# Kernel optimization log

Measured on AMD Instinct MI355X. Metric: run time of the kernel, lower is better.

## Reference

```python
import jax, jax.numpy as jnp
import numpy as np

B, N, E, H, NDIM, WS = 1, 4096, 512, 8, 16, 128


def setup_inputs() -> dict:
    key = jax.random.key(0)
    ks = jax.random.split(key, 8)
    x = jax.random.normal(ks[0], (B, N, E), jnp.float32)
    W_qkv = jax.random.normal(ks[1], (E, 3 * E), jnp.float32) * (E ** -0.5)
    b_qkv = jnp.zeros((3 * E,), jnp.float32)
    W_out = jax.random.normal(ks[2], (E, E), jnp.float32) * (E ** -0.5)
    b_out = jnp.zeros((E,), jnp.float32)
    omega = jax.random.normal(ks[3], (E,), jnp.float32)
    p_coeff = 0.1 * jax.random.normal(ks[4], (E, NDIM), jnp.float32)
    # keep |q|<1 so the 4096-step EMA recurrence is stable (original randn init diverges)
    q_coeff = jax.random.uniform(ks[5], (E, NDIM), jnp.float32, minval=-0.95, maxval=0.95)
    gamma = 0.1 * jax.random.normal(ks[6], (E, NDIM), jnp.float32)
    adaptive_weights = jnp.ones((2,), jnp.float32)
    return dict(x=x, W_qkv=W_qkv, b_qkv=b_qkv, W_out=W_out, b_out=b_out,
                omega=omega, p_coeff=p_coeff, q_coeff=q_coeff, gamma=gamma,
                adaptive_weights=adaptive_weights)


def reference(x, W_qkv, b_qkv, W_out, b_out, omega, p_coeff, q_coeff, gamma, adaptive_weights):
    b, n, e = x.shape
    dk = e // H
    # qkv projection
    qkv = x @ W_qkv + b_qkv                                # (b, n, 3e)
    q, k, v = jnp.split(qkv, 3, axis=-1)
    to_heads = lambda t: t.reshape(b, n, H, dk).transpose(0, 2, 1, 3)  # (b, h, n, dk)
    q, k, v = to_heads(q), to_heads(k), to_heads(v)
    # full QK^T (as in source) then block-local causal multiplicative mask
    dots = jnp.einsum('bhid,bhjd->bhij', q, k) * (dk ** -0.5)
    idx = jnp.arange(n)
    blk, pos = idx // WS, idx % WS
    mask = (blk[:, None] == blk[None, :]) & (pos[None, :] <= pos[:, None])
    dots = dots * mask.astype(dots.dtype)                  # scores * tril within each window block, 0 elsewhere
    attn = jax.nn.softmax(dots, axis=-1)                   # dropout is identity in eval
    out_attn = jnp.einsum('bhij,bhjd->bhid', attn, v)
    out_attn = out_attn.transpose(0, 2, 1, 3).reshape(b, n, e) @ W_out + b_out
    # CEMA: per-channel linear recurrence h_t = p*x_t + q*h_{t-1}; y_t = sum_d gamma*h_t
    # (source uses complex64 hidden but p,q,gamma,x are real -> imag part stays 0; .real == real math)
    ndim = p_coeff.shape[1]
    def step(h, xt):                                       # h: (b, e, ndim), xt: (b, e)
        h = p_coeff[None] * xt[:, :, None] + q_coeff[None] * h
        return h, jnp.sum(gamma[None] * h, axis=-1)        # (b, e)
    h0 = jnp.zeros((b, e, ndim), x.dtype)
    _, ys = jax.lax.scan(step, h0, jnp.swapaxes(x, 0, 1))  # ys: (n, b, e)
    x_cema = jnp.swapaxes(ys, 0, 1)
    w = jax.nn.softmax(adaptive_weights)
    return w[0] * out_attn + w[1] * x_cema
```

## Files before the change

kernel.cpp:

```cpp
#include <hip/hip_runtime.h>
#include <hip/hip_bf16.h>


typedef __bf16 bf16x8 __attribute__((ext_vector_type(8)));
typedef float  f32x4  __attribute__((ext_vector_type(4)));

#define N_TOK   4096
#define EDIM    512
#define DKH     64
#define WSZ     128
#define QKV_LD  1536
#define CCH     128
#define CLEN    32

__device__ __forceinline__ void glds16(const void* gsrc, void* ldst) {
  __builtin_amdgcn_global_load_lds(
      (const __attribute__((address_space(1))) void*)gsrc,
      (__attribute__((address_space(3))) void*)ldst,
      16, 0, 0);
}

template <int MODE, int BM, int BN, int WM, int WN>
__device__ __forceinline__ void gemm_body(const __bf16* __restrict__ A,
                                          const __bf16* __restrict__ Bt,
                                          const float* __restrict__ bias,
                                          __bf16* __restrict__ Cb,
                                          float* __restrict__ Cf,
                                          int K, int ldc,
                                          const float* __restrict__ cema,
                                          const float* __restrict__ aw,
                                          int bx, int by, int t) {
  __shared__ __bf16 As[BM * 32];
  __shared__ __bf16 Bs[BN * 32];
  const int lane = t & 63, wid = t >> 6;
  const int quad = lane >> 4, c16 = lane & 15;
  const int wm = (wid % (BM / WM)) * WM, wn = (wid / (BM / WM)) * WN;
  const int m0 = bx * BM, n0 = by * BN;

  f32x4 acc[WM / 16][WN / 16] = {};

  const int ar = t >> 2, ac = (t & 3) * 8;
  const __bf16* gA = A + (size_t)(m0 + ar) * K + ac;
  const __bf16* gB = Bt + (size_t)(n0 + ar) * K + ac;

  for (int k0 = 0; k0 < K; k0 += 32) {
#pragma unroll
    for (int i = 0; i < BM / 64; i++)
      glds16(gA + (size_t)i * 64 * K + k0, As + i * 2048 + t * 8);
#pragma unroll
    for (int i = 0; i < BN / 64; i++)
      glds16(gB + (size_t)i * 64 * K + k0, Bs + i * 2048 + t * 8);
    __syncthreads();
    bf16x8 af[WM / 16], bf[WN / 16];
#pragma unroll
    for (int i = 0; i < WM / 16; i++)
      af[i] = *(const bf16x8*)&As[(wm + i * 16 + c16) * 32 + quad * 8];
#pragma unroll
    for (int i = 0; i < WN / 16; i++)
      bf[i] = *(const bf16x8*)&Bs[(wn + i * 16 + c16) * 32 + quad * 8];
#pragma unroll
    for (int mi = 0; mi < WM / 16; mi++)
#pragma unroll
      for (int ni = 0; ni < WN / 16; ni++)
        acc[mi][ni] = __builtin_amdgcn_mfma_f32_16x16x32_bf16(af[mi], bf[ni], acc[mi][ni], 0, 0, 0);
    __syncthreads();
  }

  float w0 = 1.f, w1 = 0.f;
  if (MODE == 1) {
    float a0 = aw[0], a1 = aw[1];
    float mx = fmaxf(a0, a1);
    float e0 = __expf(a0 - mx), e1 = __expf(a1 - mx);
    w0 = e0 / (e0 + e1);
    w1 = 1.f - w0;
  }
#pragma unroll
  for (int mi = 0; mi < WM / 16; mi++) {
#pragma unroll
    for (int ni = 0; ni < WN / 16; ni++) {
      const int col = n0 + wn + ni * 16 + c16;
      const float bv = bias[col];
#pragma unroll
      for (int r = 0; r < 4; r++) {
        const int row = m0 + wm + mi * 16 + quad * 4 + r;
        float v = acc[mi][ni][r] + bv;
        if (MODE == 1) {
          v = w0 * v + w1 * cema[(size_t)row * EDIM + col];
          Cf[(size_t)row * ldc + col] = v;
        } else {
          Cb[(size_t)row * ldc + col] = (__bf16)v;
        }
      }
    }
  }
}

__global__ __launch_bounds__(256) void fused_prep_cemaA(const float* __restrict__ Wq,
                                                        __bf16* __restrict__ WtQ,
                                                        const float* __restrict__ Wo,
                                                        __bf16* __restrict__ WtO,
                                                        const float* __restrict__ x,
                                                        const float* __restrict__ pc,
                                                        const float* __restrict__ qc,
                                                        float* __restrict__ h_end,
                                                        __bf16* __restrict__ x_bf,
                                                        float* __restrict__ xpart) {
  const int b = blockIdx.x, t = threadIdx.x;
  if (b < 256) {
    __shared__ float tile[64][65];
    int bx = b & 31;
    const int by = b >> 5;
    const float* in;
    __bf16* out;
    int C;
    if (bx < 24) { in = Wq; out = WtQ; C = 1536; }
    else         { bx -= 24; in = Wo; out = WtO; C = 512; }
    const int R = 512;
#pragma unroll
    for (int i = 0; i < 16; i++) {
      int idx = t + i * 256;
      int r = idx >> 6, c = idx & 63;
      tile[r][c] = in[(size_t)(by * 64 + r) * C + bx * 64 + c];
    }
    __syncthreads();
#pragma unroll
    for (int i = 0; i < 16; i++) {
      int idx = t + i * 256;
      int r = idx >> 6, c = idx & 63;
      out[(size_t)(bx * 64 + r) * R + by * 64 + c] = (__bf16)tile[c][r];
    }
  } else {
    const int bb = b - 256;
    const int c = bb >> 1;
    const int e = ((bb & 1) << 8) + t;
    float p[16], q[16], h[16];
#pragma unroll
    for (int d4 = 0; d4 < 4; d4++) {
      const float4 pv = ((const float4*)(pc + e * 16))[d4];
      const float4 qv = ((const float4*)(qc + e * 16))[d4];
      p[d4 * 4 + 0] = pv.x; p[d4 * 4 + 1] = pv.y; p[d4 * 4 + 2] = pv.z; p[d4 * 4 + 3] = pv.w;
      q[d4 * 4 + 0] = qv.x; q[d4 * 4 + 1] = qv.y; q[d4 * 4 + 2] = qv.z; q[d4 * 4 + 3] = qv.w;
    }
#pragma unroll
    for (int d = 0; d < 16; d++) h[d] = 0.f;
    const float* xp = x + (size_t)c * CLEN * EDIM + e;
    __bf16* xb = x_bf + (size_t)c * CLEN * EDIM + e;
    float sx = 0.f;
#pragma unroll 4
    for (int tt = 0; tt < CLEN; tt++) {
      const float xv = xp[(size_t)tt * EDIM];
      xb[(size_t)tt * EDIM] = (__bf16)xv;
      sx += xv;
#pragma unroll
      for (int d = 0; d < 16; d++) h[d] = fmaf(p[d], xv, q[d] * h[d]);
    }
    xpart[(size_t)c * 512 + e] = sx;
    float* o = h_end + (size_t)c * 8192 + e * 16;
#pragma unroll
    for (int d = 0; d < 16; d++) o[d] = h[d];
  }
}

__global__ __launch_bounds__(256) void fused_qkv_scan_vtot(const __bf16* __restrict__ x_bf,
                                                           const __bf16* __restrict__ WtQ,
                                                           const float* __restrict__ b_qkv,
                                                           __bf16* __restrict__ qkv,
                                                           const float* __restrict__ qc,
                                                           const float* __restrict__ h_end,
                                                           float* __restrict__ hin,
                                                           float* __restrict__ T,
                                                           const float* __restrict__ xpart,
                                                           float* __restrict__ vtot) {
  const int b = blockIdx.x, t = threadIdx.x;
  if (b < 384) {
    gemm_body<0, 128, 128, 64, 64>(x_bf, WtQ, b_qkv, qkv, nullptr,
                                   EDIM, QKV_LD, nullptr, nullptr,
                                   b & 31, b >> 5, t);
  } else if (b < 640) {
    const int idx = (b - 384) * 256 + t;
    const int g = idx >> 13;
    const int i = idx & 8191;
    const float q = qc[i];
    float Q = q * q; Q = Q * Q; Q = Q * Q; Q = Q * Q; Q = Q * Q;
    float L = 0.f;
    const int c0 = g * 16;
#pragma unroll 4
    for (int j = 0; j < 16; j++) {
      hin[(size_t)(c0 + j) * 8192 + i] = L;
      L = h_end[(size_t)(c0 + j) * 8192 + i] + Q * L;
    }
    T[(size_t)g * 8192 + i] = L;
  } else {
    __shared__ float xs[512];
    float s0 = 0.f, s1 = 0.f;
    for (int c = 0; c < CCH; c++) {
      s0 += xpart[(size_t)c * 512 + t];
      s1 += xpart[(size_t)c * 512 + 256 + t];
    }
    xs[t] = s0; xs[256 + t] = s1;
    __syncthreads();
    const int wid = t >> 6, lane = t & 63;
#pragma unroll
    for (int u = 0; u < 8; u++) {
      const int c = (b - 640) * 32 + wid * 8 + u;
      const bf16x8 wv = *(const bf16x8*)(WtQ + (size_t)(1024 + c) * 512 + lane * 8);
      float s = 0.f;
#pragma unroll
      for (int z = 0; z < 8; z++) s = fmaf((float)wv[z], xs[lane * 8 + z], s);
#pragma unroll
      for (int m = 1; m < 64; m <<= 1) s += __shfl_xor(s, m);
      if (lane == 0) vtot[c] = s + (float)N_TOK * b_qkv[1024 + c];
    }
  }
}

__global__ __launch_bounds__(256) void fused_attn_cemaC(const __bf16* __restrict__ qkv,
                                                        const float* __restrict__ vtot,
                                                        __bf16* __restrict__ out_attn,
                                                        const float* __restrict__ x,
                                                        const float* __restrict__ pc,
                                                        const float* __restrict__ qc,
                                                        const float* __restrict__ gma,
                                                        const float* __restrict__ hin,
                                                        const float* __restrict__ T,
                                                        float* __restrict__ y) {
  const int b = blockIdx.x, t = threadIdx.x;
  if (b < 256) {
    __shared__ float4 smem4[3104];
    __bf16* Qs = (__bf16*)smem4;
    __bf16* Ks = (__bf16*)smem4 + 8192;
    __bf16* Ws = (__bf16*)smem4;
    __bf16* Vt = (__bf16*)smem4 + 16384;
    float* rowsum = (float*)((__bf16*)smem4 + 24576);

    const int lane = t & 63, wid = t >> 6;
    const int quad = lane >> 4, c16 = lane & 15;
    const int h = b & 7, w = b >> 3;
    const size_t base = (size_t)w * WSZ * QKV_LD + h * DKH;

    const int sr = t >> 3, sc = (t & 7) * 8;
#pragma unroll
    for (int i = 0; i < 4; i++) {
      glds16(qkv + base + (size_t)(i * 32 + sr) * QKV_LD + sc,        Qs + i * 2048 + t * 8);
      glds16(qkv + base + EDIM + (size_t)(i * 32 + sr) * QKV_LD + sc, Ks + i * 2048 + t * 8);
    }
    __syncthreads();

    const int wm = (wid & 1) * 64, wn = (wid >> 1) * 64;
    f32x4 accs[4][4] = {};
#pragma unroll
    for (int k0 = 0; k0 < DKH; k0 += 32) {
      bf16x8 af[4], bf[4];
#pragma unroll
      for (int i = 0; i < 4; i++) {
        af[i] = *(const bf16x8*)&Qs[(wm + i * 16 + c16) * DKH + k0 + quad * 8];
        bf[i] = *(const bf16x8*)&Ks[(wn + i * 16 + c16) * DKH + k0 + quad * 8];
      }
#pragma unroll
      for (int mi = 0; mi < 4; mi++)
#pragma unroll
        for (int ni = 0; ni < 4; ni++)
          accs[mi][ni] = __builtin_amdgcn_mfma_f32_16x16x32_bf16(af[mi], bf[ni], accs[mi][ni], 0, 0, 0);
    }
    __syncthreads();

    if (t < 128) rowsum[t] = 0.f;
    __syncthreads();

#pragma unroll
    for (int mi = 0; mi < 4; mi++) {
      float rs[4] = {0.f, 0.f, 0.f, 0.f};
#pragma unroll
      for (int ni = 0; ni < 4; ni++) {
        const int j = wn + ni * 16 + c16;
#pragma unroll
        for (int r = 0; r < 4; r++) {
          const int i = wm + mi * 16 + quad * 4 + r;
          const float s = accs[mi][ni][r] * 0.125f;
          const float wv = (j <= i) ? (__expf(s) - 1.f) : 0.f;
          Ws[i * 128 + j] = (__bf16)wv;
          rs[r] += wv;
        }
      }
#pragma unroll
      for (int m = 1; m < 16; m <<= 1)
#pragma unroll
        for (int r = 0; r < 4; r++) rs[r] += __shfl_xor(rs[r], m);
      if (c16 == 0) {
#pragma unroll
        for (int r = 0; r < 4; r++)
          atomicAdd(&rowsum[wm + mi * 16 + quad * 4 + r], rs[r]);
      }
    }

    {
      const int j = t & 127;
      const int dh = (t >> 7) * 32;
      const __bf16* vp = qkv + base + 2 * EDIM + (size_t)j * QKV_LD + dh;
#pragma unroll
      for (int u = 0; u < 4; u++) {
        bf16x8 vv = *(const bf16x8*)(vp + u * 8);
#pragma unroll
        for (int x2 = 0; x2 < 8; x2++) Vt[(dh + u * 8 + x2) * 128 + j] = vv[x2];
      }
    }
    __syncthreads();

    f32x4 acco[2][4] = {};
#pragma unroll
    for (int j0 = 0; j0 < 128; j0 += 32) {
      bf16x8 af2[2], bf2[4];
#pragma unroll
      for (int mi = 0; mi < 2; mi++)
        af2[mi] = *(const bf16x8*)&Ws[(wid * 32 + mi * 16 + c16) * 128 + j0 + quad * 8];
#pragma unroll
      for (int ni = 0; ni < 4; ni++)
        bf2[ni] = *(const bf16x8*)&Vt[(ni * 16 + c16) * 128 + j0 + quad * 8];
#pragma unroll
      for (int mi = 0; mi < 2; mi++)
#pragma unroll
        for (int ni = 0; ni < 4; ni++)
          acco[mi][ni] = __builtin_amdgcn_mfma_f32_16x16x32_bf16(af2[mi], bf2[ni], acco[mi][ni], 0, 0, 0);
    }

#pragma unroll
    for (int mi = 0; mi < 2; mi++) {
#pragma unroll
      for (int ni = 0; ni < 4; ni++) {
        const int d = ni * 16 + c16;
        const float vt = vtot[h * DKH + d];
#pragma unroll
        for (int r = 0; r < 4; r++) {
          const int i = wid * 32 + mi * 16 + quad * 4 + r;
          const float denom = rowsum[i] + (float)N_TOK;
          const float val = (acco[mi][ni][r] + vt) / denom;
          out_attn[(size_t)(w * WSZ + i) * EDIM + h * DKH + d] = (__bf16)val;
        }
      }
    }
  } else {
    const int bb = b - 256;
    const int c = bb >> 1;
    const int e = ((bb & 1) << 8) + t;
    const int g = c >> 4, j = c & 15;
    float p[16], q[16], gm[16], h[16], Sv[16], Q32[16], Q512[16];
#pragma unroll
    for (int d4 = 0; d4 < 4; d4++) {
      const float4 pv = ((const float4*)(pc + e * 16))[d4];
      const float4 qv = ((const float4*)(qc + e * 16))[d4];
      const float4 gv = ((const float4*)(gma + e * 16))[d4];
      p[d4 * 4 + 0] = pv.x; p[d4 * 4 + 1] = pv.y; p[d4 * 4 + 2] = pv.z; p[d4 * 4 + 3] = pv.w;
      q[d4 * 4 + 0] = qv.x; q[d4 * 4 + 1] = qv.y; q[d4 * 4 + 2] = qv.z; q[d4 * 4 + 3] = qv.w;
      gm[d4 * 4 + 0] = gv.x; gm[d4 * 4 + 1] = gv.y; gm[d4 * 4 + 2] = gv.z; gm[d4 * 4 + 3] = gv.w;
    }
#pragma unroll
    for (int d = 0; d < 16; d++) {
      float Q = q[d] * q[d]; Q = Q * Q; Q = Q * Q; Q = Q * Q; Q = Q * Q;
      Q32[d] = Q;
      float Q5 = Q * Q; Q5 = Q5 * Q5; Q5 = Q5 * Q5; Q5 = Q5 * Q5;
      Q512[d] = Q5;
      Sv[d] = 0.f;
    }
    for (int gg = 0; gg < g; gg++) {
      const float* Tp = T + (size_t)gg * 8192 + e * 16;
#pragma unroll
      for (int d = 0; d < 16; d++) Sv[d] = Tp[d] + Q512[d] * Sv[d];
    }
    const float* hi = hin + (size_t)c * 8192 + e * 16;
#pragma unroll
    for (int d = 0; d < 16; d++) {
      float Qj = 1.f;
      for (int jj = 0; jj < j; jj++) Qj *= Q32[d];
      h[d] = hi[d] + Qj * Sv[d];
    }
    const float* xp = x + (size_t)c * CLEN * EDIM + e;
    float* yp = y + (size_t)c * CLEN * EDIM + e;
#pragma unroll 4
    for (int tt = 0; tt < CLEN; tt++) {
      const float xv = xp[(size_t)tt * EDIM];
      float acc = 0.f;
#pragma unroll
      for (int d = 0; d < 16; d++) {
        h[d] = fmaf(p[d], xv, q[d] * h[d]);
        acc = fmaf(gm[d], h[d], acc);
      }
      yp[(size_t)tt * EDIM] = acc;
    }
  }
}

__global__ __launch_bounds__(256) void gemm_out_kernel(const __bf16* __restrict__ A,
                                                       const __bf16* __restrict__ Bt,
                                                       const float* __restrict__ bias,
                                                       float* __restrict__ Cf,
                                                       const float* __restrict__ cema,
                                                       const float* __restrict__ aw) {
  gemm_body<1, 64, 64, 32, 32>(A, Bt, bias, nullptr, Cf, EDIM, EDIM, cema, aw,
                               blockIdx.x, blockIdx.y, threadIdx.x);
}

extern "C" void kernel_launch(void* const* d_in, const int* in_sizes, int n_in,
                              void* d_out, int out_size, void* d_ws, size_t ws_size,
                              hipStream_t stream) {
  const float* x       = (const float*)d_in[0];
  const float* W_qkv   = (const float*)d_in[1];
  const float* b_qkv   = (const float*)d_in[2];
  const float* W_out   = (const float*)d_in[3];
  const float* b_out   = (const float*)d_in[4];
  const float* p_coeff = (const float*)d_in[6];
  const float* q_coeff = (const float*)d_in[7];
  const float* gamma   = (const float*)d_in[8];
  const float* aw      = (const float*)d_in[9];

  char* ws = (char*)d_ws;
  __bf16* qkv      = (__bf16*)(ws);
  __bf16* WtQ      = (__bf16*)(ws + 12582912);
  __bf16* WtO      = (__bf16*)(ws + 14155776);
  __bf16* out_attn = (__bf16*)(ws + 14680064);
  float*  vtot     = (float*) (ws + 18874368);
  float*  h_end    = (float*) (ws + 18876416);
  float*  hin      = (float*) (ws + 23070720);
  float*  y        = (float*) (ws + 27265024);
  __bf16* x_bf     = (__bf16*)(ws + 35653632);
  float*  Tg       = (float*) (ws + 39849984);
  float*  xpart    = (float*) (ws + 40112128);

  fused_prep_cemaA<<<512, 256, 0, stream>>>(W_qkv, WtQ, W_out, WtO,
                                            x, p_coeff, q_coeff, h_end, x_bf, xpart);

  fused_qkv_scan_vtot<<<656, 256, 0, stream>>>(x_bf, WtQ, b_qkv, qkv,
                                               q_coeff, h_end, hin, Tg, xpart, vtot);

  fused_attn_cemaC<<<512, 256, 0, stream>>>(qkv, vtot, out_attn,
                                            x, p_coeff, q_coeff, gamma, hin, Tg, y);

  gemm_out_kernel<<<dim3(64, 8), 256, 0, stream>>>(out_attn, WtO, b_out,
                                                   (float*)d_out, y, aw);
}
```

Baseline: 125.9 us.

## Fuse QKV projection into windowed attention and fold vtot term into output GEMM

The QKV GEMM now runs inside the per-window, per-head attention block. Each 512-thread workgroup computes its Q/K/V tile straight into LDS and then does QK^T, the exp-1 weighting and PV, so the 12MB qkv buffer is never written to or read back from global memory. The constant softmax term (sum of V over all tokens) is moved out of attention: the CEMA kernel computes vtot·W_out per head, and the output GEMM adds it scaled by a per-row reciprocal denominator. The CEMA inter-chunk scan becomes a flat 128-step sequential pass, replacing the two-level T/Q512 prefix, and the GEMMs gain double-buffered LDS loads. The cost is a fused kernel with only 256 heavy blocks, each using large LDS, plus a longer serial scan path.

```diff
diff --git a/kernel.cpp b/kernel.cpp
--- a/kernel.cpp
+++ b/kernel.cpp
@@ -9,7 +9,6 @@
 #define EDIM    512
 #define DKH     64
 #define WSZ     128
-#define QKV_LD  1536
 #define CCH     128
 #define CLEN    32
 
@@ -18,81 +17,6 @@
       (const __attribute__((address_space(1))) void*)gsrc,
       (__attribute__((address_space(3))) void*)ldst,
       16, 0, 0);
-}
-
-template <int MODE, int BM, int BN, int WM, int WN>
-__device__ __forceinline__ void gemm_body(const __bf16* __restrict__ A,
-                                          const __bf16* __restrict__ Bt,
-                                          const float* __restrict__ bias,
-                                          __bf16* __restrict__ Cb,
-                                          float* __restrict__ Cf,
-                                          int K, int ldc,
-                                          const float* __restrict__ cema,
-                                          const float* __restrict__ aw,
-                                          int bx, int by, int t) {
-  __shared__ __bf16 As[BM * 32];
-  __shared__ __bf16 Bs[BN * 32];
-  const int lane = t & 63, wid = t >> 6;
-  const int quad = lane >> 4, c16 = lane & 15;
-  const int wm = (wid % (BM / WM)) * WM, wn = (wid / (BM / WM)) * WN;
-  const int m0 = bx * BM, n0 = by * BN;
-
-  f32x4 acc[WM / 16][WN / 16] = {};
-
-  const int ar = t >> 2, ac = (t & 3) * 8;
-  const __bf16* gA = A + (size_t)(m0 + ar) * K + ac;
-  const __bf16* gB = Bt + (size_t)(n0 + ar) * K + ac;
-
-  for (int k0 = 0; k0 < K; k0 += 32) {
-#pragma unroll
-    for (int i = 0; i < BM / 64; i++)
-      glds16(gA + (size_t)i * 64 * K + k0, As + i * 2048 + t * 8);
-#pragma unroll
-    for (int i = 0; i < BN / 64; i++)
-      glds16(gB + (size_t)i * 64 * K + k0, Bs + i * 2048 + t * 8);
-    __syncthreads();
-    bf16x8 af[WM / 16], bf[WN / 16];
-#pragma unroll
-    for (int i = 0; i < WM / 16; i++)
-      af[i] = *(const bf16x8*)&As[(wm + i * 16 + c16) * 32 + quad * 8];
-#pragma unroll
-    for (int i = 0; i < WN / 16; i++)
-      bf[i] = *(const bf16x8*)&Bs[(wn + i * 16 + c16) * 32 + quad * 8];
-#pragma unroll
-    for (int mi = 0; mi < WM / 16; mi++)
-#pragma unroll
-      for (int ni = 0; ni < WN / 16; ni++)
-        acc[mi][ni] = __builtin_amdgcn_mfma_f32_16x16x32_bf16(af[mi], bf[ni], acc[mi][ni], 0, 0, 0);
-    __syncthreads();
-  }
-
-  float w0 = 1.f, w1 = 0.f;
-  if (MODE == 1) {
-    float a0 = aw[0], a1 = aw[1];
-    float mx = fmaxf(a0, a1);
-    float e0 = __expf(a0 - mx), e1 = __expf(a1 - mx);
-    w0 = e0 / (e0 + e1);
-    w1 = 1.f - w0;
-  }
-#pragma unroll
-  for (int mi = 0; mi < WM / 16; mi++) {
-#pragma unroll
-    for (int ni = 0; ni < WN / 16; ni++) {
-      const int col = n0 + wn + ni * 16 + c16;
-      const float bv = bias[col];
-#pragma unroll
-      for (int r = 0; r < 4; r++) {
-        const int row = m0 + wm + mi * 16 + quad * 4 + r;
-        float v = acc[mi][ni][r] + bv;
-        if (MODE == 1) {
-          v = w0 * v + w1 * cema[(size_t)row * EDIM + col];
-          Cf[(size_t)row * ldc + col] = v;
-        } else {
-          Cb[(size_t)row * ldc + col] = (__bf16)v;
-        }
-      }
-    }
-  }
 }
 
 __global__ __launch_bounds__(256) void fused_prep_cemaA(const float* __restrict__ Wq,
@@ -161,189 +85,205 @@
   }
 }
 
-__global__ __launch_bounds__(256) void fused_qkv_scan_vtot(const __bf16* __restrict__ x_bf,
-                                                           const __bf16* __restrict__ WtQ,
-                                                           const float* __restrict__ b_qkv,
-                                                           __bf16* __restrict__ qkv,
-                                                           const float* __restrict__ qc,
-                                                           const float* __restrict__ h_end,
-                                                           float* __restrict__ hin,
-                                                           float* __restrict__ T,
-                                                           const float* __restrict__ xpart,
-                                                           float* __restrict__ vtot) {
-  const int b = blockIdx.x, t = threadIdx.x;
-  if (b < 384) {
-    gemm_body<0, 128, 128, 64, 64>(x_bf, WtQ, b_qkv, qkv, nullptr,
-                                   EDIM, QKV_LD, nullptr, nullptr,
-                                   b & 31, b >> 5, t);
-  } else if (b < 640) {
-    const int idx = (b - 384) * 256 + t;
-    const int g = idx >> 13;
-    const int i = idx & 8191;
+__global__ __launch_bounds__(512) void fused_qkv_attn_scanB(const __bf16* __restrict__ x_bf,
+                                                            const __bf16* __restrict__ WtQ,
+                                                            const float* __restrict__ b_qkv,
+                                                            const float* __restrict__ qc,
+                                                            const float* __restrict__ h_end,
+                                                            float* __restrict__ hin,
+                                                            __bf16* __restrict__ out_attn,
+                                                            float* __restrict__ rd) {
+  const int B = blockIdx.x, t = threadIdx.x;
+  __shared__ f32x4 smemv[3680];
+  if (B >= 256) {
+    const int i = (B - 256) * 512 + t;
     const float q = qc[i];
     float Q = q * q; Q = Q * Q; Q = Q * Q; Q = Q * Q; Q = Q * Q;
     float L = 0.f;
-    const int c0 = g * 16;
 #pragma unroll 4
-    for (int j = 0; j < 16; j++) {
-      hin[(size_t)(c0 + j) * 8192 + i] = L;
-      L = h_end[(size_t)(c0 + j) * 8192 + i] + Q * L;
-    }
-    T[(size_t)g * 8192 + i] = L;
-  } else {
-    __shared__ float xs[512];
-    float s0 = 0.f, s1 = 0.f;
-    for (int c = 0; c < CCH; c++) {
-      s0 += xpart[(size_t)c * 512 + t];
-      s1 += xpart[(size_t)c * 512 + 256 + t];
-    }
-    xs[t] = s0; xs[256 + t] = s1;
+    for (int c = 0; c < 128; c++) {
+      hin[(size_t)c * 8192 + i] = L;
+      L = h_end[(size_t)c * 8192 + i] + Q * L;
+    }
+    return;
+  }
+  char* sb = (char*)smemv;
+  const int lane = t & 63, wid = t >> 6;
+  const int quad = lane >> 4, c16 = lane & 15;
+  const int xcd = B & 7, h = (B >> 3) & 7, wg = B >> 6;
+  const int w = wg * 8 + xcd;
+
+  __bf16* AsP[2] = {(__bf16*)sb, (__bf16*)(sb + 20480)};
+  __bf16* BsP[2] = {(__bf16*)(sb + 8192), (__bf16*)(sb + 28672)};
+
+  const int wm = (wid & 3) * 32, wc = (wid >> 2) * 96;
+  f32x4 acc[2][6] = {};
+  const int ar = t >> 2, ac8 = (t & 3) * 8;
+  const __bf16* gA = x_bf + (size_t)(w * 128 + ar) * 512 + ac8;
+  const int grB0 = (ar < 64) ? (h * 64 + ar) : (512 + h * 64 + (ar - 64));
+  const __bf16* gB0 = WtQ + (size_t)grB0 * 512 + ac8;
+  const __bf16* gB1 = WtQ + (size_t)(1024 + h * 64 + ar) * 512 + ac8;
+
+  glds16(gA, AsP[0] + t * 8);
+  glds16(gB0, BsP[0] + t * 8);
+  if (wid < 4) glds16(gB1, BsP[0] + 4096 + t * 8);
+  __syncthreads();
+
+  int cur = 0;
+  for (int k0 = 0; k0 < 512; k0 += 32) {
+    if (k0 + 32 < 512) {
+      glds16(gA + k0 + 32, AsP[cur ^ 1] + t * 8);
+      glds16(gB0 + k0 + 32, BsP[cur ^ 1] + t * 8);
+      if (wid < 4) glds16(gB1 + k0 + 32, BsP[cur ^ 1] + 4096 + t * 8);
+    }
+    bf16x8 af[2], bfr[6];
+#pragma unroll
+    for (int i = 0; i < 2; i++)
+      af[i] = *(const bf16x8*)&AsP[cur][(wm + i * 16 + c16) * 32 + quad * 8];
+#pragma unroll
+    for (int j = 0; j < 6; j++)
+      bfr[j] = *(const bf16x8*)&BsP[cur][(wc + j * 16 + c16) * 32 + quad * 8];
+#pragma unroll
+    for (int mi = 0; mi < 2; mi++)
+#pragma unroll
+      for (int ni = 0; ni < 6; ni++)
+        acc[mi][ni] = __builtin_amdgcn_mfma_f32_16x16x32_bf16(af[mi], bfr[ni], acc[mi][ni], 0, 0, 0);
     __syncthreads();
-    const int wid = t >> 6, lane = t & 63;
-#pragma unroll
-    for (int u = 0; u < 8; u++) {
-      const int c = (b - 640) * 32 + wid * 8 + u;
-      const bf16x8 wv = *(const bf16x8*)(WtQ + (size_t)(1024 + c) * 512 + lane * 8);
-      float s = 0.f;
-#pragma unroll
-      for (int z = 0; z < 8; z++) s = fmaf((float)wv[z], xs[lane * 8 + z], s);
-#pragma unroll
-      for (int m = 1; m < 64; m <<= 1) s += __shfl_xor(s, m);
-      if (lane == 0) vtot[c] = s + (float)N_TOK * b_qkv[1024 + c];
-    }
-  }
-}
-
-__global__ __launch_bounds__(256) void fused_attn_cemaC(const __bf16* __restrict__ qkv,
-                                                        const float* __restrict__ vtot,
-                                                        __bf16* __restrict__ out_attn,
-                                                        const float* __restrict__ x,
-                                                        const float* __restrict__ pc,
-                                                        const float* __restrict__ qc,
-                                                        const float* __restrict__ gma,
-                                                        const float* __restrict__ hin,
-                                                        const float* __restrict__ T,
-                                                        float* __restrict__ y) {
+    cur ^= 1;
+  }
+
+  __bf16* Qs = (__bf16*)sb;
+  __bf16* Ks = (__bf16*)(sb + 18432);
+  __bf16* Vt = (__bf16*)(sb + 40960);
+  __bf16* Ws = (__bf16*)sb;
+  float* rowsum = (float*)(sb + 58368);
+
+#pragma unroll
+  for (int ni = 0; ni < 6; ni++) {
+    const int cc = wc + ni * 16 + c16;
+    const int g = cc >> 6;
+    const int d = cc & 63;
+    const float bv = b_qkv[g * 512 + h * 64 + d];
+#pragma unroll
+    for (int mi = 0; mi < 2; mi++)
+#pragma unroll
+      for (int r = 0; r < 4; r++) {
+        const int row = wm + mi * 16 + quad * 4 + r;
+        const float v = acc[mi][ni][r] + bv;
+        if (g == 0)      Qs[row * 72 + d] = (__bf16)v;
+        else if (g == 1) Ks[row * 72 + d] = (__bf16)v;
+        else             Vt[d * 136 + row] = (__bf16)v;
+      }
+  }
+  __syncthreads();
+
+  const int swm = (wid & 1) * 64, swn = (wid >> 1) * 32;
+  f32x4 accs[4][2] = {};
+#pragma unroll
+  for (int k0 = 0; k0 < DKH; k0 += 32) {
+    bf16x8 af2[4], bf2[2];
+#pragma unroll
+    for (int i = 0; i < 4; i++)
+      af2[i] = *(const bf16x8*)&Qs[(swm + i * 16 + c16) * 72 + k0 + quad * 8];
+#pragma unroll
+    for (int j = 0; j < 2; j++)
+      bf2[j] = *(const bf16x8*)&Ks[(swn + j * 16 + c16) * 72 + k0 + quad * 8];
+#pragma unroll
+    for (int mi = 0; mi < 4; mi++)
+#pragma unroll
+      for (int ni = 0; ni < 2; ni++)
+        accs[mi][ni] = __builtin_amdgcn_mfma_f32_16x16x32_bf16(af2[mi], bf2[ni], accs[mi][ni], 0, 0, 0);
+  }
+  __syncthreads();
+  if (t < 128) rowsum[t] = 0.f;
+  __syncthreads();
+
+#pragma unroll
+  for (int mi = 0; mi < 4; mi++) {
+    float rs[4] = {0.f, 0.f, 0.f, 0.f};
+#pragma unroll
+    for (int ni = 0; ni < 2; ni++) {
+      const int j = swn + ni * 16 + c16;
+#pragma unroll
+      for (int r = 0; r < 4; r++) {
+        const int i = swm + mi * 16 + quad * 4 + r;
+        const float s = accs[mi][ni][r] * 0.125f;
+        const float wv = (j <= i) ? (__expf(s) - 1.f) : 0.f;
+        Ws[i * 136 + j] = (__bf16)wv;
+        rs[r] += wv;
+      }
+    }
+#pragma unroll
+    for (int m = 1; m < 16; m <<= 1)
+#pragma unroll
+      for (int r = 0; r < 4; r++) rs[r] += __shfl_xor(rs[r], m);
+    if (c16 == 0) {
+#pragma unroll
+      for (int r = 0; r < 4; r++)
+        atomicAdd(&rowsum[swm + mi * 16 + quad * 4 + r], rs[r]);
+    }
+  }
+  __syncthreads();
+
+  const int pwm = (wid & 3) * 32, pwn = (wid >> 2) * 32;
+  f32x4 acco[2][2] = {};
+#pragma unroll
+  for (int j0 = 0; j0 < 128; j0 += 32) {
+    bf16x8 af3[2], bf3[2];
+#pragma unroll
+    for (int mi = 0; mi < 2; mi++)
+      af3[mi] = *(const bf16x8*)&Ws[(pwm + mi * 16 + c16) * 136 + j0 + quad * 8];
+#pragma unroll
+    for (int ni = 0; ni < 2; ni++)
+      bf3[ni] = *(const bf16x8*)&Vt[(pwn + ni * 16 + c16) * 136 + j0 + quad * 8];
+#pragma unroll
+    for (int mi = 0; mi < 2; mi++)
+#pragma unroll
+      for (int ni = 0; ni < 2; ni++)
+        acco[mi][ni] = __builtin_amdgcn_mfma_f32_16x16x32_bf16(af3[mi], bf3[ni], acco[mi][ni], 0, 0, 0);
+  }
+
+#pragma unroll
+  for (int mi = 0; mi < 2; mi++)
+#pragma unroll
+    for (int ni = 0; ni < 2; ni++) {
+      const int d = pwn + ni * 16 + c16;
+#pragma unroll
+      for (int r = 0; r < 4; r++) {
+        const int i = pwm + mi * 16 + quad * 4 + r;
+        const float denom = rowsum[i] + (float)N_TOK;
+        out_attn[(size_t)(w * 128 + i) * EDIM + h * 64 + d] = (__bf16)(acco[mi][ni][r] / denom);
+      }
+    }
+  if ((wid >> 2) == 0 && c16 == 0) {
+#pragma unroll
+    for (int mi = 0; mi < 2; mi++)
+#pragma unroll
+      for (int r = 0; r < 4; r++) {
+        const int i = pwm + mi * 16 + quad * 4 + r;
+        rd[(size_t)(w * 128 + i) * 8 + h] = 1.f / (rowsum[i] + (float)N_TOK);
+      }
+  }
+}
+
+__global__ __launch_bounds__(256) void fused_cemaC_vtW(const float* __restrict__ x,
+                                                       const float* __restrict__ pc,
+                                                       const float* __restrict__ qc,
+                                                       const float* __restrict__ gma,
+                                                       const float* __restrict__ hin,
+                                                       float* __restrict__ y,
+                                                       const float* __restrict__ xpart,
+                                                       const __bf16* __restrict__ WtQ,
+                                                       const float* __restrict__ b_qkv,
+                                                       const float* __restrict__ W_out,
+                                                       float* __restrict__ vtWoH) {
   const int b = blockIdx.x, t = threadIdx.x;
+  __shared__ float xsL[512];
+  __shared__ float vtL[64];
   if (b < 256) {
-    __shared__ float4 smem4[3104];
-    __bf16* Qs = (__bf16*)smem4;
-    __bf16* Ks = (__bf16*)smem4 + 8192;
-    __bf16* Ws = (__bf16*)smem4;
-    __bf16* Vt = (__bf16*)smem4 + 16384;
-    float* rowsum = (float*)((__bf16*)smem4 + 24576);
-
-    const int lane = t & 63, wid = t >> 6;
-    const int quad = lane >> 4, c16 = lane & 15;
-    const int h = b & 7, w = b >> 3;
-    const size_t base = (size_t)w * WSZ * QKV_LD + h * DKH;
-
-    const int sr = t >> 3, sc = (t & 7) * 8;
-#pragma unroll
-    for (int i = 0; i < 4; i++) {
-      glds16(qkv + base + (size_t)(i * 32 + sr) * QKV_LD + sc,        Qs + i * 2048 + t * 8);
-      glds16(qkv + base + EDIM + (size_t)(i * 32 + sr) * QKV_LD + sc, Ks + i * 2048 + t * 8);
-    }
-    __syncthreads();
-
-    const int wm = (wid & 1) * 64, wn = (wid >> 1) * 64;
-    f32x4 accs[4][4] = {};
-#pragma unroll
-    for (int k0 = 0; k0 < DKH; k0 += 32) {
-      bf16x8 af[4], bf[4];
-#pragma unroll
-      for (int i = 0; i < 4; i++) {
-        af[i] = *(const bf16x8*)&Qs[(wm + i * 16 + c16) * DKH + k0 + quad * 8];
-        bf[i] = *(const bf16x8*)&Ks[(wn + i * 16 + c16) * DKH + k0 + quad * 8];
-      }
-#pragma unroll
-      for (int mi = 0; mi < 4; mi++)
-#pragma unroll
-        for (int ni = 0; ni < 4; ni++)
-          accs[mi][ni] = __builtin_amdgcn_mfma_f32_16x16x32_bf16(af[mi], bf[ni], accs[mi][ni], 0, 0, 0);
-    }
-    __syncthreads();
-
-    if (t < 128) rowsum[t] = 0.f;
-    __syncthreads();
-
-#pragma unroll
-    for (int mi = 0; mi < 4; mi++) {
-      float rs[4] = {0.f, 0.f, 0.f, 0.f};
-#pragma unroll
-      for (int ni = 0; ni < 4; ni++) {
-        const int j = wn + ni * 16 + c16;
-#pragma unroll
-        for (int r = 0; r < 4; r++) {
-          const int i = wm + mi * 16 + quad * 4 + r;
-          const float s = accs[mi][ni][r] * 0.125f;
-          const float wv = (j <= i) ? (__expf(s) - 1.f) : 0.f;
-          Ws[i * 128 + j] = (__bf16)wv;
-          rs[r] += wv;
-        }
-      }
-#pragma unroll
-      for (int m = 1; m < 16; m <<= 1)
-#pragma unroll
-        for (int r = 0; r < 4; r++) rs[r] += __shfl_xor(rs[r], m);
-      if (c16 == 0) {
-#pragma unroll
-        for (int r = 0; r < 4; r++)
-          atomicAdd(&rowsum[wm + mi * 16 + quad * 4 + r], rs[r]);
-      }
-    }
-
-    {
-      const int j = t & 127;
-      const int dh = (t >> 7) * 32;
-      const __bf16* vp = qkv + base + 2 * EDIM + (size_t)j * QKV_LD + dh;
-#pragma unroll
-      for (int u = 0; u < 4; u++) {
-        bf16x8 vv = *(const bf16x8*)(vp + u * 8);
-#pragma unroll
-        for (int x2 = 0; x2 < 8; x2++) Vt[(dh + u * 8 + x2) * 128 + j] = vv[x2];
-      }
-    }
-    __syncthreads();
-
-    f32x4 acco[2][4] = {};
-#pragma unroll
-    for (int j0 = 0; j0 < 128; j0 += 32) {
-      bf16x8 af2[2], bf2[4];
-#pragma unroll
-      for (int mi = 0; mi < 2; mi++)
-        af2[mi] = *(const bf16x8*)&Ws[(wid * 32 + mi * 16 + c16) * 128 + j0 + quad * 8];
-#pragma unroll
-      for (int ni = 0; ni < 4; ni++)
-        bf2[ni] = *(const bf16x8*)&Vt[(ni * 16 + c16) * 128 + j0 + quad * 8];
-#pragma unroll
-      for (int mi = 0; mi < 2; mi++)
-#pragma unroll
-        for (int ni = 0; ni < 4; ni++)
-          acco[mi][ni] = __builtin_amdgcn_mfma_f32_16x16x32_bf16(af2[mi], bf2[ni], acco[mi][ni], 0, 0, 0);
-    }
-
-#pragma unroll
-    for (int mi = 0; mi < 2; mi++) {
-#pragma unroll
-      for (int ni = 0; ni < 4; ni++) {
-        const int d = ni * 16 + c16;
-        const float vt = vtot[h * DKH + d];
-#pragma unroll
-        for (int r = 0; r < 4; r++) {
-          const int i = wid * 32 + mi * 16 + quad * 4 + r;
-          const float denom = rowsum[i] + (float)N_TOK;
-          const float val = (acco[mi][ni][r] + vt) / denom;
-          out_attn[(size_t)(w * WSZ + i) * EDIM + h * DKH + d] = (__bf16)val;
-        }
-      }
-    }
-  } else {
-    const int bb = b - 256;
-    const int c = bb >> 1;
-    const int e = ((bb & 1) << 8) + t;
-    const int g = c >> 4, j = c & 15;
-    float p[16], q[16], gm[16], h[16], Sv[16], Q32[16], Q512[16];
+    const int c = b >> 1;
+    const int e = ((b & 1) << 8) + t;
+    float p[16], q[16], gm[16], hreg[16];
 #pragma unroll
     for (int d4 = 0; d4 < 4; d4++) {
       const float4 pv = ((const float4*)(pc + e * 16))[d4];
@@ -353,26 +293,9 @@
       q[d4 * 4 + 0] = qv.x; q[d4 * 4 + 1] = qv.y; q[d4 * 4 + 2] = qv.z; q[d4 * 4 + 3] = qv.w;
       gm[d4 * 4 + 0] = gv.x; gm[d4 * 4 + 1] = gv.y; gm[d4 * 4 + 2] = gv.z; gm[d4 * 4 + 3] = gv.w;
     }
-#pragma unroll
-    for (int d = 0; d < 16; d++) {
-      float Q = q[d] * q[d]; Q = Q * Q; Q = Q * Q; Q = Q * Q; Q = Q * Q;
-      Q32[d] = Q;
-      float Q5 = Q * Q; Q5 = Q5 * Q5; Q5 = Q5 * Q5; Q5 = Q5 * Q5;
-      Q512[d] = Q5;
-      Sv[d] = 0.f;
-    }
-    for (int gg = 0; gg < g; gg++) {
-      const float* Tp = T + (size_t)gg * 8192 + e * 16;
-#pragma unroll
-      for (int d = 0; d < 16; d++) Sv[d] = Tp[d] + Q512[d] * Sv[d];
-    }
     const float* hi = hin + (size_t)c * 8192 + e * 16;
 #pragma unroll
-    for (int d = 0; d < 16; d++) {
-      float Qj = 1.f;
-      for (int jj = 0; jj < j; jj++) Qj *= Q32[d];
-      h[d] = hi[d] + Qj * Sv[d];
-    }
+    for (int d = 0; d < 16; d++) hreg[d] = hi[d];
     const float* xp = x + (size_t)c * CLEN * EDIM + e;
     float* yp = y + (size_t)c * CLEN * EDIM + e;
 #pragma unroll 4
@@ -381,10 +304,41 @@
       float acc = 0.f;
 #pragma unroll
       for (int d = 0; d < 16; d++) {
-        h[d] = fmaf(p[d], xv, q[d] * h[d]);
-        acc = fmaf(gm[d], h[d], acc);
+        hreg[d] = fmaf(p[d], xv, q[d] * hreg[d]);
+        acc = fmaf(gm[d], hreg[d], acc);
       }
       yp[(size_t)tt * EDIM] = acc;
+    }
+  } else {
+    const int h = b - 256;
+    float s0 = 0.f, s1 = 0.f;
+    for (int c = 0; c < CCH; c++) {
+      s0 += xpart[(size_t)c * 512 + t];
+      s1 += xpart[(size_t)c * 512 + 256 + t];
+    }
+    xsL[t] = s0; xsL[256 + t] = s1;
+    __syncthreads();
+    const int wid = t >> 6, lane = t & 63;
+#pragma unroll
+    for (int u = 0; u < 16; u++) {
+      const int c = wid * 16 + u;
+      const bf16x8 wv = *(const bf16x8*)(WtQ + (size_t)(1024 + h * 64 + c) * 512 + lane * 8);
+      float s = 0.f;
+#pragma unroll
+      for (int z = 0; z < 8; z++) s = fmaf((float)wv[z], xsL[lane * 8 + z], s);
+#pragma unroll
+      for (int m = 1; m < 64; m <<= 1) s += __shfl_xor(s, m);
+      if (lane == 0) vtL[c] = s + (float)N_TOK * b_qkv[1024 + h * 64 + c];
+    }
+    __syncthreads();
+#pragma unroll
+    for (int oo = 0; oo < 2; oo++) {
+      const int o = oo * 256 + t;
+      float accv = 0.f;
+#pragma unroll 8
+      for (int d = 0; d < 64; d++)
+        accv = fmaf(vtL[d], W_out[(size_t)(h * 64 + d) * 512 + o], accv);
+      vtWoH[(size_t)h * 512 + o] = accv;
     }
   }
 }
@@ -394,9 +348,76 @@
                                                        const float* __restrict__ bias,
                                                        float* __restrict__ Cf,
                                                        const float* __restrict__ cema,
-                                                       const float* __restrict__ aw) {
-  gemm_body<1, 64, 64, 32, 32>(A, Bt, bias, nullptr, Cf, EDIM, EDIM, cema, aw,
-                               blockIdx.x, blockIdx.y, threadIdx.x);
+                                                       const float* __restrict__ aw,
+                                                       const float* __restrict__ rd,
+                                                       const float* __restrict__ vtWoH) {
+  __shared__ __bf16 AsB[2][64 * 32];
+  __shared__ __bf16 BsB[2][64 * 32];
+  const int t = threadIdx.x;
+  const int lane = t & 63, wid = t >> 6;
+  const int quad = lane >> 4, c16 = lane & 15;
+  const int wm = (wid & 1) * 32, wn = (wid >> 1) * 32;
+  const int m0 = blockIdx.x * 64, n0 = blockIdx.y * 64;
+  f32x4 acc[2][2] = {};
+  const int ar = t >> 2, ac8 = (t & 3) * 8;
+  const __bf16* gA = A + (size_t)(m0 + ar) * EDIM + ac8;
+  const __bf16* gB = Bt + (size_t)(n0 + ar) * EDIM + ac8;
+
+  glds16(gA, AsB[0] + t * 8);
+  glds16(gB, BsB[0] + t * 8);
+  __syncthreads();
+  int cur = 0;
+  for (int k0 = 0; k0 < EDIM; k0 += 32) {
+    if (k0 + 32 < EDIM) {
+      glds16(gA + k0 + 32, AsB[cur ^ 1] + t * 8);
+      glds16(gB + k0 + 32, BsB[cur ^ 1] + t * 8);
+    }
+    bf16x8 af[2], bfr[2];
+#pragma unroll
+    for (int i = 0; i < 2; i++) {
+      af[i] = *(const bf16x8*)&AsB[cur][(wm + i * 16 + c16) * 32 + quad * 8];
+      bfr[i] = *(const bf16x8*)&BsB[cur][(wn + i * 16 + c16) * 32 + quad * 8];
+    }
+#pragma unroll
+    for (int mi = 0; mi < 2; mi++)
+#pragma unroll
+      for (int ni = 0; ni < 2; ni++)
+        acc[mi][ni] = __builtin_amdgcn_mfma_f32_16x16x32_bf16(af[mi], bfr[ni], acc[mi][ni], 0, 0, 0);
+    __syncthreads();
+    cur ^= 1;
+  }
+
+  const float a0 = aw[0], a1 = aw[1];
+  const float mx = fmaxf(a0, a1);
+  const float e0 = __expf(a0 - mx), e1 = __expf(a1 - mx);
+  const float w0 = e0 / (e0 + e1);
+  const float w1 = 1.f - w0;
+
+  float vw[2][8];
+#pragma unroll
+  for (int ni = 0; ni < 2; ni++) {
+    const int col = n0 + wn + ni * 16 + c16;
+#pragma unroll
+    for (int hh = 0; hh < 8; hh++) vw[ni][hh] = vtWoH[(size_t)hh * 512 + col];
+  }
+#pragma unroll
+  for (int mi = 0; mi < 2; mi++) {
+#pragma unroll
+    for (int r = 0; r < 4; r++) {
+      const int row = m0 + wm + mi * 16 + quad * 4 + r;
+      const float4 rp0 = *(const float4*)(rd + (size_t)row * 8);
+      const float4 rp1 = *(const float4*)(rd + (size_t)row * 8 + 4);
+#pragma unroll
+      for (int ni = 0; ni < 2; ni++) {
+        const int col = n0 + wn + ni * 16 + c16;
+        float v = acc[mi][ni][r] + bias[col];
+        v += rp0.x * vw[ni][0] + rp0.y * vw[ni][1] + rp0.z * vw[ni][2] + rp0.w * vw[ni][3]
+           + rp1.x * vw[ni][4] + rp1.y * vw[ni][5] + rp1.z * vw[ni][6] + rp1.w * vw[ni][7];
+        v = w0 * v + w1 * cema[(size_t)row * EDIM + col];
+        Cf[(size_t)row * EDIM + col] = v;
+      }
+    }
+  }
 }
 
 extern "C" void kernel_launch(void* const* d_in, const int* in_sizes, int n_in,
@@ -413,27 +434,26 @@
   const float* aw      = (const float*)d_in[9];
 
   char* ws = (char*)d_ws;
-  __bf16* qkv      = (__bf16*)(ws);
-  __bf16* WtQ      = (__bf16*)(ws + 12582912);
-  __bf16* WtO      = (__bf16*)(ws + 14155776);
-  __bf16* out_attn = (__bf16*)(ws + 14680064);
-  float*  vtot     = (float*) (ws + 18874368);
-  float*  h_end    = (float*) (ws + 18876416);
-  float*  hin      = (float*) (ws + 23070720);
-  float*  y        = (float*) (ws + 27265024);
-  __bf16* x_bf     = (__bf16*)(ws + 35653632);
-  float*  Tg       = (float*) (ws + 39849984);
-  float*  xpart    = (float*) (ws + 40112128);
+  __bf16* WtQ      = (__bf16*)(ws);
+  __bf16* WtO      = (__bf16*)(ws + 1572864);
+  __bf16* x_bf     = (__bf16*)(ws + 2097152);
+  float*  h_end    = (float*) (ws + 6291456);
+  float*  hin      = (float*) (ws + 10485760);
+  float*  xpart    = (float*) (ws + 14680064);
+  __bf16* out_attn = (__bf16*)(ws + 14942208);
+  float*  rd       = (float*) (ws + 19136512);
+  float*  vtWoH    = (float*) (ws + 19267584);
+  float*  y        = (float*) (ws + 19283968);
 
   fused_prep_cemaA<<<512, 256, 0, stream>>>(W_qkv, WtQ, W_out, WtO,
                                             x, p_coeff, q_coeff, h_end, x_bf, xpart);
 
-  fused_qkv_scan_vtot<<<656, 256, 0, stream>>>(x_bf, WtQ, b_qkv, qkv,
-                                               q_coeff, h_end, hin, Tg, xpart, vtot);
-
-  fused_attn_cemaC<<<512, 256, 0, stream>>>(qkv, vtot, out_attn,
-                                            x, p_coeff, q_coeff, gamma, hin, Tg, y);
+  fused_qkv_attn_scanB<<<272, 512, 0, stream>>>(x_bf, WtQ, b_qkv, q_coeff,
+                                                h_end, hin, out_attn, rd);
+
+  fused_cemaC_vtW<<<264, 256, 0, stream>>>(x, p_coeff, q_coeff, gamma, hin, y,
+                                           xpart, WtQ, b_qkv, W_out, vtWoH);
 
   gemm_out_kernel<<<dim3(64, 8), 256, 0, stream>>>(out_attn, WtO, b_out,
-                                                   (float*)d_out, y, aw);
-}
+                                                   (float*)d_out, y, aw, rd, vtWoH);
+}
```

New measurement: 142.2 us. 12.9% more time.
